# Kernel optimization log

Hardware: AMD Instinct MI355X
Metric: run time of the kernel (lower is better)

The kernel has to match this reference:

```python
import jax, jax.numpy as jnp
import numpy as np

M_MARGIN = 0.25
GAMMA = 64.0
EPS = 1e-5


def _circle_loss_one_way(enc, dec):
    # enc, dec: [N, D]. Faithful to the torch rotate-concat construction:
    # cos_sim[j, k] = cosine(enc[j], dec[(j + k) % N]); column 0 is the positive.
    N = enc.shape[0]
    dot = enc @ dec.T                                   # [N, N]
    en = jnp.sqrt(jnp.sum(enc * enc, axis=1, keepdims=True))   # [N, 1]
    dn = jnp.sqrt(jnp.sum(dec * dec, axis=1, keepdims=True))   # [N, 1]
    S = dot / (en * dn.T + EPS)                         # [N, N] cosine sims
    r = jnp.arange(N)
    idx = (r[:, None] + r[None, :]) % N                 # [N, N] rolled column index
    cos_sim = jnp.take_along_axis(S, idx, axis=1)       # [N, N]
    sp = cos_sim[:, 0:1]                                # [N, 1] positives (diag of S)
    sn = cos_sim[:, 1:]                                 # [N, N-1] negatives
    ap = jnp.maximum(-jax.lax.stop_gradient(sp) + 1.0 + M_MARGIN, 0.0)
    an = jnp.maximum(jax.lax.stop_gradient(sn) + M_MARGIN, 0.0)
    delta_p = 1.0 - M_MARGIN
    delta_n = M_MARGIN
    logit_p = -ap * (sp - delta_p) * GAMMA              # [N, 1]
    logit_n = an * (sn - delta_n) * GAMMA               # [N, N-1]
    lse_n = jax.nn.logsumexp(logit_n, axis=0)           # [N-1]
    lse_p = jax.nn.logsumexp(logit_p, axis=0)           # [1] (cols of repeated sp are identical)
    return jax.nn.softplus(lse_n + lse_p)               # [N-1]


def reference(encoder_output, decoder_output):
    loss_a = _circle_loss_one_way(encoder_output, decoder_output)
    loss_b = _circle_loss_one_way(decoder_output, encoder_output)
    return jnp.mean((loss_a + loss_b) / 2.0)


def setup_inputs() -> dict:
    key = jax.random.key(0)
    k1, k2 = jax.random.split(key)
    N, D = 8192, 128
    return {
        "encoder_output": jax.random.normal(k1, (N, D), dtype=jnp.float32),
        "decoder_output": jax.random.normal(k2, (N, D), dtype=jnp.float32),
    }
```

## Files before the change

kernel.cpp:

```cpp
#include <hip/hip_runtime.h>
#include <hip/hip_bf16.h>

#define NN 8192

using bf16x8 = __attribute__((ext_vector_type(8))) short;
using f32x4  = __attribute__((ext_vector_type(4))) float;

__device__ __forceinline__ void gl_lds16(const void* g, void* l) {
  __builtin_amdgcn_global_load_lds(
      (const __attribute__((address_space(1))) unsigned int*)(unsigned long long)g,
      (__attribute__((address_space(3))) unsigned int*)(unsigned int)(unsigned long long)l,
      16, 0, 0);
}

__global__ __launch_bounds__(256) void k_prep(const float* __restrict__ enc,
                                              const float* __restrict__ dec,
                                              unsigned* __restrict__ Abf,
                                              unsigned* __restrict__ Bbf,
                                              float* __restrict__ logit_p,
                                              float* __restrict__ bandsum) {
  const int t = threadIdx.x;
  const int l16 = t & 15;
  const int row = blockIdx.x * 16 + (t >> 4);
  const int tid = blockIdx.x * 256 + t;
  if (tid < 64 * 256) bandsum[tid] = 0.0f;

  const float4* e4 = reinterpret_cast<const float4*>(enc) + (size_t)row * 32 + l16 * 2;
  const float4* d4 = reinterpret_cast<const float4*>(dec) + (size_t)row * 32 + l16 * 2;
  float4 e0 = e4[0], e1 = e4[1];
  float4 d0 = d4[0], d1 = d4[1];

  float se = e0.x*e0.x + e0.y*e0.y + e0.z*e0.z + e0.w*e0.w
           + e1.x*e1.x + e1.y*e1.y + e1.z*e1.z + e1.w*e1.w;
  float sd = d0.x*d0.x + d0.y*d0.y + d0.z*d0.z + d0.w*d0.w
           + d1.x*d1.x + d1.y*d1.y + d1.z*d1.z + d1.w*d1.w;
  float sp = e0.x*d0.x + e0.y*d0.y + e0.z*d0.z + e0.w*d0.w
           + e1.x*d1.x + e1.y*d1.y + e1.z*d1.z + e1.w*d1.w;
#pragma unroll
  for (int off = 1; off < 16; off <<= 1) {
    se += __shfl_xor(se, off);
    sd += __shfl_xor(sd, off);
    sp += __shfl_xor(sp, off);
  }
  float ie = rsqrtf(se), id = rsqrtf(sd);

  union { __hip_bfloat162 h; unsigned u; } p;
  uint4 ua, ub;
  p.h = __float22bfloat162_rn(make_float2(e0.x * ie, e0.y * ie)); ua.x = p.u;
  p.h = __float22bfloat162_rn(make_float2(e0.z * ie, e0.w * ie)); ua.y = p.u;
  p.h = __float22bfloat162_rn(make_float2(e1.x * ie, e1.y * ie)); ua.z = p.u;
  p.h = __float22bfloat162_rn(make_float2(e1.z * ie, e1.w * ie)); ua.w = p.u;
  p.h = __float22bfloat162_rn(make_float2(d0.x * id, d0.y * id)); ub.x = p.u;
  p.h = __float22bfloat162_rn(make_float2(d0.z * id, d0.w * id)); ub.y = p.u;
  p.h = __float22bfloat162_rn(make_float2(d1.x * id, d1.y * id)); ub.z = p.u;
  p.h = __float22bfloat162_rn(make_float2(d1.z * id, d1.w * id)); ub.w = p.u;
  reinterpret_cast<uint4*>(Abf)[(size_t)row * 16 + l16] = ua;
  reinterpret_cast<uint4*>(Bbf)[(size_t)row * 16 + l16] = ub;

  if (l16 == 0) {
    float en = se * ie, dn = sd * id;
    float s  = sp / (en * dn + 1e-5f);
    logit_p[row] = -fmaxf(1.25f - s, 0.0f) * (s - 0.75f) * 64.0f;
  }
}

__global__ __launch_bounds__(256, 2) void k_main(const unsigned short* __restrict__ A,
                                                 const unsigned short* __restrict__ B,
                                                 float* __restrict__ bandsum) {
  __shared__ __align__(16) unsigned short As[128 * 128];
  __shared__ __align__(16) unsigned short Bs[128 * 128];
  __shared__ float part[4][256];

  const int t  = threadIdx.x;
  const int T  = blockIdx.x;
  const int sp = blockIdx.y;

#pragma unroll
  for (int q = 0; q < 4; ++q) part[q][t] = 0.0f;

  const int lane = t & 63;
  const int w = t >> 6, wrow = w >> 1, wcol = w & 1;
  const int l15 = lane & 15, quad = lane >> 4;
  const int x7 = l15 & 7;

  const unsigned short* Abase = As + (wrow * 64 + l15) * 128;
  const unsigned short* Bbase = Bs + (wcol * 64 + l15) * 128;
  char* AsB = (char*)As;
  char* BsB = (char*)Bs;

  float dreg[28];
#pragma unroll
  for (int i = 0; i < 28; ++i) dreg[i] = 0.0f;

  const int rl_lo = t >> 4;
  const int cch   = t & 15;
  {
    const int by = sp * 8;
    const int bx = (by + T) & 63;
    const char* Ag = (const char*)(A + (size_t)by * 128 * 128);
    const char* Bg = (const char*)(B + (size_t)bx * 128 * 128);
#pragma unroll
    for (int j = 0; j < 8; ++j) {
      int rl   = j * 16 + rl_lo;
      int c    = cch ^ (rl & 7);
      int goff = rl * 256 + c * 16;
      int loff = j * 4096 + t * 16;
      gl_lds16(Ag + goff, AsB + loff);
      gl_lds16(Bg + goff, BsB + loff);
    }
  }
  __syncthreads();

  for (int it = 0; it < 8; ++it) {
    f32x4 acc[4][4];
    const f32x4 zv = {0.f, 0.f, 0.f, 0.f};
#pragma unroll
    for (int r = 0; r < 4; ++r)
#pragma unroll
      for (int c = 0; c < 4; ++c) acc[r][c] = zv;

#pragma unroll
    for (int ks = 0; ks < 4; ++ks) {
      bf16x8 a[4], b[4];
      const int off = ((ks * 4 + quad) ^ x7) * 8;
#pragma unroll
      for (int r = 0; r < 4; ++r)
        a[r] = *reinterpret_cast<const bf16x8*>(Abase + r * 16 * 128 + off);
#pragma unroll
      for (int c = 0; c < 4; ++c)
        b[c] = *reinterpret_cast<const bf16x8*>(Bbase + c * 16 * 128 + off);
#pragma unroll
      for (int r = 0; r < 4; ++r)
#pragma unroll
        for (int c = 0; c < 4; ++c)
          acc[r][c] = __builtin_amdgcn_mfma_f32_16x16x32_bf16(a[r], b[c], acc[r][c], 0, 0, 0);
    }

    __syncthreads();

    if (it < 7) {
      const int by = sp * 8 + it + 1;
      const int bx = (by + T) & 63;
      const char* Ag = (const char*)(A + (size_t)by * 128 * 128);
      const char* Bg = (const char*)(B + (size_t)bx * 128 * 128);
#pragma unroll
      for (int j = 0; j < 8; ++j) {
        int rl   = j * 16 + rl_lo;
        int c    = cch ^ (rl & 7);
        int goff = rl * 256 + c * 16;
        int loff = j * 4096 + t * 16;
        gl_lds16(Ag + goff, AsB + loff);
        gl_lds16(Bg + goff, BsB + loff);
      }
    }

#pragma unroll
    for (int dlt = -3; dlt <= 3; ++dlt) {
#pragma unroll
      for (int g = 0; g < 4; ++g) {
        float s = 0.0f;
#pragma unroll
        for (int r = 0; r < 4; ++r) {
          int c = r + dlt;
          if (c < 0 || c > 3) continue;
          float sn = acc[r][c][g];
          float an = fmaxf(sn + 0.25f, 0.0f);
          float u  = fmaf(sn, 92.332483f, -23.083121f);
          s += exp2f(an * u);
        }
        dreg[(dlt + 3) * 4 + g] += s;
      }
    }

    __syncthreads();
  }

  const int  Qoff = (wcol - wrow) * 64 + 127;
  const int  v    = l15 - quad * 4;
  const bool leader = (quad == 0) || (l15 <= 3);
  const bool ok1 = (l15 <= 11) && (quad <= 2);
  const bool ok2 = (l15 <= 7)  && (quad <= 1);

#pragma unroll
  for (int dlt = -3; dlt <= 3; ++dlt) {
#pragma unroll
    for (int g = 0; g < 4; ++g) {
      float s = dreg[(dlt + 3) * 4 + g];
      float t1 = __shfl_down(s, 20); s += ok1 ? t1 : 0.0f;
      float t2 = __shfl_down(s, 40); s += ok2 ? t2 : 0.0f;
      int ld = Qoff + dlt * 16 - g + v;
      if (leader) unsafeAtomicAdd(&part[w][ld], s);
    }
  }
  __syncthreads();

  if (t < 255) {
    float vv = part[0][t] + part[1][t] + part[2][t] + part[3][t];
    unsafeAtomicAdd(&bandsum[T * 256 + t], vv);
  }
}

__global__ __launch_bounds__(1024) void k_fin(const float* __restrict__ logit_p,
                                              const float* __restrict__ bandsum,
                                              float* __restrict__ out) {
  __shared__ float sm[16];
  const int t = threadIdx.x, lane = t & 63, w = t >> 6;

  float m = -3.0e38f;
  for (int i = t; i < NN; i += 1024) m = fmaxf(m, logit_p[i]);
#pragma unroll
  for (int off = 32; off; off >>= 1) m = fmaxf(m, __shfl_down(m, off));
  if (lane == 0) sm[w] = m;
  __syncthreads();
  m = sm[0];
#pragma unroll
  for (int k = 1; k < 16; ++k) m = fmaxf(m, sm[k]);
  __syncthreads();

  float s = 0.0f;
  for (int i = t; i < NN; i += 1024) s += __expf(logit_p[i] - m);
#pragma unroll
  for (int off = 32; off; off >>= 1) s += __shfl_down(s, off);
  if (lane == 0) sm[w] = s;
  __syncthreads();
  s = 0.0f;
#pragma unroll
  for (int k = 0; k < 16; ++k) s += sm[k];
  float lse_p = m + __logf(s);
  __syncthreads();

  float acc = 0.0f;
  for (int d = t; d < NN; d += 1024) {
    if (d == 0) continue;
    int Ta = d >> 7;
    float se = bandsum[Ta * 256 + (d & 127) + 127];
    if (d & 127) {
      int Tb = (Ta + 1) & 63;
      se += bandsum[Tb * 256 + (d & 127) - 1];
    }
    float x = __logf(se) + lse_p;
    acc += fmaxf(x, 0.0f) + __logf(1.0f + __expf(-fabsf(x)));
  }
#pragma unroll
  for (int off = 32; off; off >>= 1) acc += __shfl_down(acc, off);
  if (lane == 0) sm[w] = acc;
  __syncthreads();
  if (t == 0) {
    float tot = 0.0f;
#pragma unroll
    for (int k = 0; k < 16; ++k) tot += sm[k];
    out[0] = tot * (1.0f / 8191.0f);
  }
}

extern "C" void kernel_launch(void* const* d_in, const int* in_sizes, int n_in,
                              void* d_out, int out_size, void* d_ws, size_t ws_size,
                              hipStream_t stream) {
  const float* enc = (const float*)d_in[0];
  const float* dec = (const float*)d_in[1];
  float* ws = (float*)d_ws;

  float*    logit_p = ws;
  float*    bandsum = ws + 8192;
  unsigned* Abf     = (unsigned*)(ws + 8192 + 16384);
  unsigned* Bbf     = Abf + 524288;
  float* out = (float*)d_out;

  k_prep<<<NN / 16, 256, 0, stream>>>(enc, dec, Abf, Bbf, logit_p, bandsum);
  dim3 grid(64, 8);
  k_main<<<grid, 256, 0, stream>>>((const unsigned short*)Abf, (const unsigned short*)Bbf, bandsum);
  k_fin<<<1, 1024, 0, stream>>>(logit_p, bandsum, out);
}
```

Before: 108.2 us.

## Fuse final reduction into main kernel via last-block counter; use hardware exp2

```diff
diff --git a/kernel.cpp b/kernel.cpp
--- a/kernel.cpp
+++ b/kernel.cpp
@@ -5,6 +5,12 @@
 
 using bf16x8 = __attribute__((ext_vector_type(8))) short;
 using f32x4  = __attribute__((ext_vector_type(4))) float;
+
+#if __has_builtin(__builtin_amdgcn_exp2f)
+#define EXP2(x) __builtin_amdgcn_exp2f(x)
+#else
+#define EXP2(x) __expf((x) * 0.69314718056f)
+#endif
 
 __device__ __forceinline__ void gl_lds16(const void* g, void* l) {
   __builtin_amdgcn_global_load_lds(
@@ -18,12 +24,14 @@
                                               unsigned* __restrict__ Abf,
                                               unsigned* __restrict__ Bbf,
                                               float* __restrict__ logit_p,
-                                              float* __restrict__ bandsum) {
+                                              float* __restrict__ bandsum,
+                                              unsigned* __restrict__ counter) {
   const int t = threadIdx.x;
   const int l16 = t & 15;
   const int row = blockIdx.x * 16 + (t >> 4);
   const int tid = blockIdx.x * 256 + t;
   if (tid < 64 * 256) bandsum[tid] = 0.0f;
+  if (tid == 64 * 256) *counter = 0u;
 
   const float4* e4 = reinterpret_cast<const float4*>(enc) + (size_t)row * 32 + l16 * 2;
   const float4* d4 = reinterpret_cast<const float4*>(dec) + (size_t)row * 32 + l16 * 2;
@@ -66,10 +74,14 @@
 
 __global__ __launch_bounds__(256, 2) void k_main(const unsigned short* __restrict__ A,
                                                  const unsigned short* __restrict__ B,
-                                                 float* __restrict__ bandsum) {
+                                                 float* __restrict__ bandsum,
+                                                 const float* __restrict__ logit_p,
+                                                 unsigned* __restrict__ counter,
+                                                 float* __restrict__ out) {
   __shared__ __align__(16) unsigned short As[128 * 128];
   __shared__ __align__(16) unsigned short Bs[128 * 128];
   __shared__ float part[4][256];
+  __shared__ unsigned lastFlag;
 
   const int t  = threadIdx.x;
   const int T  = blockIdx.x;
@@ -93,20 +105,18 @@
   for (int i = 0; i < 28; ++i) dreg[i] = 0.0f;
 
   const int rl_lo = t >> 4;
-  const int cch   = t & 15;
+  const int lgoff = rl_lo * 256 + ((t & 15) ^ (rl_lo & 7)) * 16;
+  const int lloff = t * 16;
+
   {
     const int by = sp * 8;
     const int bx = (by + T) & 63;
-    const char* Ag = (const char*)(A + (size_t)by * 128 * 128);
-    const char* Bg = (const char*)(B + (size_t)bx * 128 * 128);
+    const char* AgT = (const char*)A + (size_t)by * 32768 + lgoff;
+    const char* BgT = (const char*)B + (size_t)bx * 32768 + lgoff;
 #pragma unroll
     for (int j = 0; j < 8; ++j) {
-      int rl   = j * 16 + rl_lo;
-      int c    = cch ^ (rl & 7);
-      int goff = rl * 256 + c * 16;
-      int loff = j * 4096 + t * 16;
-      gl_lds16(Ag + goff, AsB + loff);
-      gl_lds16(Bg + goff, BsB + loff);
+      gl_lds16(AgT + j * 4096, AsB + lloff + j * 4096);
+      gl_lds16(BgT + j * 4096, BsB + lloff + j * 4096);
     }
   }
   __syncthreads();
@@ -141,16 +151,12 @@
     if (it < 7) {
       const int by = sp * 8 + it + 1;
       const int bx = (by + T) & 63;
-      const char* Ag = (const char*)(A + (size_t)by * 128 * 128);
-      const char* Bg = (const char*)(B + (size_t)bx * 128 * 128);
+      const char* AgT = (const char*)A + (size_t)by * 32768 + lgoff;
+      const char* BgT = (const char*)B + (size_t)bx * 32768 + lgoff;
 #pragma unroll
       for (int j = 0; j < 8; ++j) {
-        int rl   = j * 16 + rl_lo;
-        int c    = cch ^ (rl & 7);
-        int goff = rl * 256 + c * 16;
-        int loff = j * 4096 + t * 16;
-        gl_lds16(Ag + goff, AsB + loff);
-        gl_lds16(Bg + goff, BsB + loff);
+        gl_lds16(AgT + j * 4096, AsB + lloff + j * 4096);
+        gl_lds16(BgT + j * 4096, BsB + lloff + j * 4096);
       }
     }
 
@@ -166,7 +172,7 @@
           float sn = acc[r][c][g];
           float an = fmaxf(sn + 0.25f, 0.0f);
           float u  = fmaf(sn, 92.332483f, -23.083121f);
-          s += exp2f(an * u);
+          s += EXP2(an * u);
         }
         dreg[(dlt + 3) * 4 + g] += s;
       }
@@ -198,39 +204,37 @@
     float vv = part[0][t] + part[1][t] + part[2][t] + part[3][t];
     unsafeAtomicAdd(&bandsum[T * 256 + t], vv);
   }
-}
-
-__global__ __launch_bounds__(1024) void k_fin(const float* __restrict__ logit_p,
-                                              const float* __restrict__ bandsum,
-                                              float* __restrict__ out) {
-  __shared__ float sm[16];
-  const int t = threadIdx.x, lane = t & 63, w = t >> 6;
+
+  __threadfence();
+  __syncthreads();
+  if (t == 0) lastFlag = (atomicAdd(counter, 1u) == 511u) ? 1u : 0u;
+  __syncthreads();
+  if (!lastFlag) return;
+
+  __threadfence();
+  float* sm = part[0];
 
   float m = -3.0e38f;
-  for (int i = t; i < NN; i += 1024) m = fmaxf(m, logit_p[i]);
+  for (int i = t; i < NN; i += 256) m = fmaxf(m, logit_p[i]);
 #pragma unroll
   for (int off = 32; off; off >>= 1) m = fmaxf(m, __shfl_down(m, off));
   if (lane == 0) sm[w] = m;
   __syncthreads();
-  m = sm[0];
-#pragma unroll
-  for (int k = 1; k < 16; ++k) m = fmaxf(m, sm[k]);
+  m = fmaxf(fmaxf(sm[0], sm[1]), fmaxf(sm[2], sm[3]));
   __syncthreads();
 
   float s = 0.0f;
-  for (int i = t; i < NN; i += 1024) s += __expf(logit_p[i] - m);
+  for (int i = t; i < NN; i += 256) s += __expf(logit_p[i] - m);
 #pragma unroll
   for (int off = 32; off; off >>= 1) s += __shfl_down(s, off);
   if (lane == 0) sm[w] = s;
   __syncthreads();
-  s = 0.0f;
-#pragma unroll
-  for (int k = 0; k < 16; ++k) s += sm[k];
+  s = sm[0] + sm[1] + sm[2] + sm[3];
   float lse_p = m + __logf(s);
   __syncthreads();
 
   float acc = 0.0f;
-  for (int d = t; d < NN; d += 1024) {
+  for (int d = t; d < NN; d += 256) {
     if (d == 0) continue;
     int Ta = d >> 7;
     float se = bandsum[Ta * 256 + (d & 127) + 127];
@@ -245,12 +249,7 @@
   for (int off = 32; off; off >>= 1) acc += __shfl_down(acc, off);
   if (lane == 0) sm[w] = acc;
   __syncthreads();
-  if (t == 0) {
-    float tot = 0.0f;
-#pragma unroll
-    for (int k = 0; k < 16; ++k) tot += sm[k];
-    out[0] = tot * (1.0f / 8191.0f);
-  }
+  if (t == 0) out[0] = (sm[0] + sm[1] + sm[2] + sm[3]) * (1.0f / 8191.0f);
 }
 
 extern "C" void kernel_launch(void* const* d_in, const int* in_sizes, int n_in,
@@ -262,12 +261,13 @@
 
   float*    logit_p = ws;
   float*    bandsum = ws + 8192;
-  unsigned* Abf     = (unsigned*)(ws + 8192 + 16384);
+  unsigned* counter = (unsigned*)(ws + 8192 + 16384);
+  unsigned* Abf     = (unsigned*)(ws + 8192 + 16384 + 256);
   unsigned* Bbf     = Abf + 524288;
-  float* out = (float*)d_out;
-
-  k_prep<<<NN / 16, 256, 0, stream>>>(enc, dec, Abf, Bbf, logit_p, bandsum);
+  float*    out     = (float*)d_out;
+
+  k_prep<<<NN / 16, 256, 0, stream>>>(enc, dec, Abf, Bbf, logit_p, bandsum, counter);
   dim3 grid(64, 8);
-  k_main<<<grid, 256, 0, stream>>>((const unsigned short*)Abf, (const unsigned short*)Bbf, bandsum);
-  k_fin<<<1, 1024, 0, stream>>>(logit_p, bandsum, out);
-}
+  k_main<<<grid, 256, 0, stream>>>((const unsigned short*)Abf, (const unsigned short*)Bbf,
+                                   bandsum, logit_p, counter, out);
+}
```

Result: slower. 144.8 us (+33.9%).
